# Kernel tuning notes

Hardware: AMD Instinct MI355X
Metric: run time of the kernel (lower is better)

The kernel has to match this reference:

```python
import jax, jax.numpy as jnp
import numpy as np

B, S, H = 8, 8192, 1024
CAPACITY_FACTOR = 0.5


def setup_inputs() -> dict:
    key = jax.random.key(0)
    ks = jax.random.split(key, 5)
    sc = lambda fan: np.float32(1.0 / np.sqrt(fan))
    return {
        "x": jax.random.normal(ks[0], (B, S, H), dtype=jnp.float32),
        # router: Linear(H, H//4) -> ReLU -> Linear(H//4, 1)
        "W1": jax.random.normal(ks[1], (H, H // 4), dtype=jnp.float32) * sc(H),
        "b1": jnp.zeros((H // 4,), dtype=jnp.float32),
        "W2": jax.random.normal(ks[2], (H // 4, 1), dtype=jnp.float32) * sc(H // 4),
        "b2": jnp.zeros((1,), dtype=jnp.float32),
        # external layer_fn realized as a dense layer: gelu(x @ Wl)
        "Wl": jax.random.normal(ks[3], (H, H), dtype=jnp.float32) * sc(H),
    }


def reference(x, W1, b1, W2, b2, Wl):
    # router scores [B, S, 1]
    scores = jax.nn.relu(jnp.einsum("bsh,hd->bsd", x, W1) + b1)
    scores = jnp.einsum("bsd,do->bso", scores, W2) + b2
    routing_weights = jax.nn.sigmoid(scores)  # [B, S, 1]

    # eval path: process only top-capacity tokens per batch row
    capacity = int(S * CAPACITY_FACTOR)
    _, top_idx = jax.lax.top_k(scores[..., 0], capacity)  # [B, C]

    selected = jnp.take_along_axis(x, top_idx[..., None], axis=1)  # [B, C, H]
    processed = jax.nn.gelu(jnp.einsum("bch,hd->bcd", selected, Wl))  # layer_fn

    batch_idx = jnp.arange(x.shape[0])[:, None]  # [B, 1]
    output = x.at[batch_idx, top_idx].set(processed)  # scatter back into clone of x
    return output, routing_weights
```

## Files before the change

### kernel.cpp

```cpp
#include <hip/hip_runtime.h>
#include <stdint.h>

#define B_   8
#define S_   8192
#define H_   1024
#define HQ_  256
#define CAP_ 4096
#define UCAP_ (S_-CAP_)
#define M_   (B_*CAP_)
#define EPSB 0.012f
#define LCAP 8192

using f32x4 = __attribute__((ext_vector_type(4))) float;
using s16x8 = __attribute__((ext_vector_type(8))) short;

__device__ __forceinline__ unsigned short f2bf(float f) {
  unsigned u = __float_as_uint(f);
  u += 0x7FFF + ((u >> 16) & 1);
  return (unsigned short)(u >> 16);
}
__device__ __forceinline__ float bf2f(unsigned short h) {
  return __uint_as_float(((unsigned)h) << 16);
}

__device__ __forceinline__ float gelu_f(float v) {
  float s = v + 0.044715f * v * v * v;
  float e = __expf(-1.5957691216057308f * s);
  return v * __builtin_amdgcn_rcpf(1.0f + e);
}

__device__ __forceinline__ unsigned mono(float f) {
  unsigned u = __float_as_uint(f);
  return (u & 0x80000000u) ? ~u : (u | 0x80000000u);
}
__device__ __forceinline__ float unmono(unsigned k) {
  unsigned u = (k & 0x80000000u) ? (k & 0x7fffffffu) : ~k;
  return __uint_as_float(u);
}

__device__ __forceinline__ void gload_lds16(const void* g, void* l) {
  __builtin_amdgcn_global_load_lds(
      (const __attribute__((address_space(1))) void*)(uintptr_t)g,
      (__attribute__((address_space(3))) void*)(uintptr_t)l,
      16, 0, 0);
}

__global__ __launch_bounds__(256) void prep_w1_kernel(
    const float* __restrict__ W1, unsigned short* __restrict__ w1t_hi) {
  __shared__ float tile[32][33];
  const int n0 = blockIdx.x * 32, k0 = blockIdx.y * 32;
  const int tx = threadIdx.x, ty = threadIdx.y;
  for (int i = ty; i < 32; i += 8) tile[i][tx] = W1[(size_t)(k0 + i) * HQ_ + n0 + tx];
  __syncthreads();
  for (int i = ty; i < 32; i += 8)
    w1t_hi[(size_t)(n0 + i) * H_ + k0 + tx] = f2bf(tile[tx][i]);
}

__global__ __launch_bounds__(512) void router_mfma_kernel(
    const float* __restrict__ x, const unsigned short* __restrict__ w1t_hi,
    const float* __restrict__ b1, const float* __restrict__ W2,
    const float* __restrict__ b2, float* __restrict__ scores,
    float* __restrict__ rw) {
  __shared__ __align__(16) unsigned short AsH[128 * 64];
  __shared__ __align__(16) unsigned short BsH[256 * 64];
  __shared__ float part[128][4];
  const int t = threadIdx.x;
  const int lane = t & 63, w = t >> 6;
  const int m0 = blockIdx.x * 128;
  const int wr = w >> 2, wc = w & 3;
  const int r16 = lane & 15, ks = lane >> 4;

  const float* aptr[4];
  int aso[4];
  #pragma unroll
  for (int u = 0; u < 4; ++u) {
    int idx = t + u * 512;
    int row = idx >> 4, q = idx & 15;
    aptr[u] = x + (size_t)(m0 + row) * H_ + q * 4;
    aso[u] = row * 64 + (((q >> 1) ^ (row & 7)) << 3) + (q & 1) * 4;
  }
  const unsigned short* bptr[4];
  int bdst[4];
  #pragma unroll
  for (int u = 0; u < 4; ++u) {
    int c0 = u * 512 + w * 64;
    int c = c0 + lane;
    int row = c >> 3, sl = c & 7;
    int slz = sl ^ (row & 7);
    bptr[u] = w1t_hi + (size_t)row * H_ + slz * 8;
    bdst[u] = c0 * 8;
  }

  f32x4 acc[4][4];
  #pragma unroll
  for (int i = 0; i < 4; ++i)
    #pragma unroll
    for (int j = 0; j < 4; ++j) acc[i][j] = (f32x4){0.f, 0.f, 0.f, 0.f};

  for (int k0 = 0; k0 < H_; k0 += 64) {
    float4 av[4];
    #pragma unroll
    for (int u = 0; u < 4; ++u) av[u] = *(const float4*)(aptr[u] + k0);
    #pragma unroll
    for (int u = 0; u < 4; ++u) gload_lds16(bptr[u] + k0, &BsH[bdst[u]]);
    #pragma unroll
    for (int u = 0; u < 4; ++u) {
      ushort4 hh;
      hh.x = f2bf(av[u].x); hh.y = f2bf(av[u].y);
      hh.z = f2bf(av[u].z); hh.w = f2bf(av[u].w);
      *(ushort4*)&AsH[aso[u]] = hh;
    }
    __syncthreads();
    #pragma unroll
    for (int kk = 0; kk < 2; ++kk) {
      const int g = kk * 4 + ks;
      s16x8 ah[4], bh[4];
      #pragma unroll
      for (int i = 0; i < 4; ++i) {
        int r = wr * 64 + i * 16 + r16;
        ah[i] = *(const s16x8*)&AsH[r * 64 + (g ^ (r & 7)) * 8];
      }
      #pragma unroll
      for (int j = 0; j < 4; ++j) {
        int r = wc * 64 + j * 16 + r16;
        bh[j] = *(const s16x8*)&BsH[r * 64 + (g ^ (r & 7)) * 8];
      }
      #pragma unroll
      for (int i = 0; i < 4; ++i)
        #pragma unroll
        for (int j = 0; j < 4; ++j)
          acc[i][j] = __builtin_amdgcn_mfma_f32_16x16x32_bf16(ah[i], bh[j], acc[i][j], 0, 0, 0);
    }
    __syncthreads();
  }

  float b1v[4], w2v[4];
  #pragma unroll
  for (int j = 0; j < 4; ++j) {
    int n = wc * 64 + j * 16 + r16;
    b1v[j] = b1[n]; w2v[j] = W2[n];
  }
  const int g4 = lane >> 4;
  #pragma unroll
  for (int i = 0; i < 4; ++i) {
    #pragma unroll
    for (int r = 0; r < 4; ++r) {
      float p = 0.f;
      #pragma unroll
      for (int j = 0; j < 4; ++j) {
        float h = acc[i][j][r] + b1v[j];
        h = fmaxf(h, 0.f);
        p = fmaf(h, w2v[j], p);
      }
      p += __shfl_xor(p, 1);
      p += __shfl_xor(p, 2);
      p += __shfl_xor(p, 4);
      p += __shfl_xor(p, 8);
      if (r16 == 0) part[wr * 64 + i * 16 + g4 * 4 + r][wc] = p;
    }
  }
  __syncthreads();
  if (t < 128) {
    float sc = part[t][0] + part[t][1] + part[t][2] + part[t][3] + b2[0];
    scores[m0 + t] = sc;
    rw[m0 + t] = 1.f / (1.f + expf(-sc));
  }
}

__global__ __launch_bounds__(1024) void select_kernel(
    const float* __restrict__ scores, float* __restrict__ thr) {
  __shared__ unsigned hist[2048];
  __shared__ unsigned sh_b, sh_gt;
  const int b = blockIdx.x;
  const int tid = threadIdx.x;
  const float* srow = scores + (size_t)b * S_;
  unsigned prefix = 0; int plen = 0; unsigned rank = CAP_;
  #pragma unroll
  for (int round = 0; round < 3; ++round) {
    const int nb = (round < 2) ? 11 : 10;
    hist[tid] = 0; hist[tid + 1024] = 0;
    __syncthreads();
    for (int i = tid; i < S_; i += 1024) {
      unsigned k = mono(srow[i]);
      if (plen == 0 || (k >> (32 - plen)) == prefix) {
        unsigned bucket = (k << plen) >> (32 - nb);
        atomicAdd(&hist[bucket], 1u);
      }
    }
    __syncthreads();
    for (int s = 1; s < 2048; s <<= 1) {
      unsigned t0 = (tid + s < 2048) ? hist[tid + s] : 0;
      unsigned t1 = (tid + 1024 + s < 2048) ? hist[tid + 1024 + s] : 0;
      __syncthreads();
      hist[tid] += t0; hist[tid + 1024] += t1;
      __syncthreads();
    }
    #pragma unroll
    for (int h = 0; h < 2; ++h) {
      int i = tid + h * 1024;
      unsigned ge = hist[i];
      unsigned gt = (i < 2047) ? hist[i + 1] : 0;
      if (gt < rank && rank <= ge) { sh_b = (unsigned)i; sh_gt = gt; }
    }
    __syncthreads();
    prefix = (prefix << nb) | sh_b;
    plen += nb;
    rank -= sh_gt;
    __syncthreads();
  }
  if (tid == 0) thr[b] = unmono(prefix);
}

__global__ __launch_bounds__(256) void band_kernel(
    const float* __restrict__ scores, const float* __restrict__ thr,
    int* __restrict__ list, int* __restrict__ count) {
  int i = blockIdx.x * 256 + threadIdx.x;
  float s = scores[i];
  int b = i >> 13;
  if (fabsf(s - thr[b]) <= EPSB) {
    int p = atomicAdd(count, 1);
    if (p < LCAP) list[p] = i;
  }
}

__global__ __launch_bounds__(256) void recompute_kernel(
    const float* __restrict__ x, const float* __restrict__ W1,
    const float* __restrict__ b1, const float* __restrict__ W2,
    const float* __restrict__ b2, const int* __restrict__ list,
    const int* __restrict__ count, float* __restrict__ scores,
    float* __restrict__ rw) {
  __shared__ float xr[4][H_];
  __shared__ float red[4][4];
  int n = *count; if (n > LCAP) n = LCAP;
  const int j = threadIdx.x;
  for (int base = blockIdx.x * 4; base < n; base += gridDim.x * 4) {
    int nt = n - base; if (nt > 4) nt = 4;
    for (int tt = 0; tt < 4; ++tt) {
      int tok = list[base + ((tt < nt) ? tt : 0)];
      const float* xrow = x + (size_t)tok * H_;
      for (int k = j; k < H_; k += 256) xr[tt][k] = xrow[k];
    }
    __syncthreads();
    float a0 = 0.f, a1 = 0.f, a2 = 0.f, a3 = 0.f;
    for (int k = 0; k < H_; ++k) {
      float wv = W1[(size_t)k * HQ_ + j];
      a0 = fmaf(xr[0][k], wv, a0);
      a1 = fmaf(xr[1][k], wv, a1);
      a2 = fmaf(xr[2][k], wv, a2);
      a3 = fmaf(xr[3][k], wv, a3);
    }
    float aa[4] = {a0, a1, a2, a3};
    #pragma unroll
    for (int tt = 0; tt < 4; ++tt) {
      float h = fmaxf(aa[tt] + b1[j], 0.f);
      float v = h * W2[j];
      v += __shfl_xor(v, 1);  v += __shfl_xor(v, 2);  v += __shfl_xor(v, 4);
      v += __shfl_xor(v, 8);  v += __shfl_xor(v, 16); v += __shfl_xor(v, 32);
      if ((j & 63) == 0) red[tt][j >> 6] = v;
    }
    __syncthreads();
    if (j < nt) {
      int tok = list[base + j];
      float sc = red[j][0] + red[j][1] + red[j][2] + red[j][3] + b2[0];
      scores[tok] = sc;
      rw[tok] = 1.f / (1.f + expf(-sc));
    }
    __syncthreads();
  }
}

__global__ __launch_bounds__(1024) void compact_kernel(
    const float* __restrict__ scores, const float* __restrict__ thr,
    int* __restrict__ comp, int* __restrict__ ucomp) {
  __shared__ int wc_eq[16], wc_sel[16], red[16];
  const int b = blockIdx.x;
  const float T = thr[b];
  const float* srow = scores + (size_t)b * S_;
  const int tid = threadIdx.x, lane = tid & 63, wid = tid >> 6;

  int cgt = 0;
  #pragma unroll
  for (int c = 0; c < 8; ++c) cgt += (srow[c * 1024 + tid] > T) ? 1 : 0;
  cgt += __shfl_xor(cgt, 1);  cgt += __shfl_xor(cgt, 2);  cgt += __shfl_xor(cgt, 4);
  cgt += __shfl_xor(cgt, 8);  cgt += __shfl_xor(cgt, 16); cgt += __shfl_xor(cgt, 32);
  if (lane == 0) red[wid] = cgt;
  __syncthreads();
  int cnt_gt = 0;
  #pragma unroll
  for (int i = 0; i < 16; ++i) cnt_gt += red[i];
  const int need = CAP_ - cnt_gt;

  int* crow = comp + b * CAP_;
  int* urow = ucomp + b * UCAP_;
  int sel_base = 0, unsel_base = 0, eq_base = 0;
  __syncthreads();
  for (int c = 0; c < 8; ++c) {
    int idx = c * 1024 + tid;
    float s = srow[idx];
    bool gt = s > T, eq = (s == T);
    unsigned long long meq = __ballot(eq);
    if (lane == 0) wc_eq[wid] = __popcll(meq);
    __syncthreads();
    int eq_off = eq_base, eq_tot = 0;
    #pragma unroll
    for (int w2 = 0; w2 < 16; ++w2) { if (w2 < wid) eq_off += wc_eq[w2]; eq_tot += wc_eq[w2]; }
    int eqpos = eq_off + __popcll(meq & ((1ull << lane) - 1));
    bool take = gt || (eq && eqpos < need);
    unsigned long long mt = __ballot(take);
    if (lane == 0) wc_sel[wid] = __popcll(mt);
    __syncthreads();
    int sel_off = sel_base, sel_tot = 0;
    #pragma unroll
    for (int w2 = 0; w2 < 16; ++w2) { if (w2 < wid) sel_off += wc_sel[w2]; sel_tot += wc_sel[w2]; }
    if (take) {
      crow[sel_off + __popcll(mt & ((1ull << lane) - 1))] = idx;
    } else {
      int un_off = unsel_base + wid * 64 - (sel_off - sel_base);
      urow[un_off + __popcll(~mt & ((1ull << lane) - 1))] = idx;
    }
    sel_base += sel_tot; unsel_base += 1024 - sel_tot; eq_base += eq_tot;
    __syncthreads();
  }
}

__global__ __launch_bounds__(256) void copy_unsel_kernel(
    const float* __restrict__ x, const int* __restrict__ ucomp,
    float* __restrict__ out) {
  int i = blockIdx.x;
  int b = i >> 12, r = i & (UCAP_ - 1);
  int token = ucomp[b * UCAP_ + r];
  size_t row = (size_t)b * S_ + token;
  const float4* src = (const float4*)(x + row * H_);
  float4* dst = (float4*)(out + row * H_);
  dst[threadIdx.x] = src[threadIdx.x];
}

__global__ __launch_bounds__(256) void wlt_kernel(
    const float* __restrict__ wl, unsigned short* __restrict__ wlt) {
  __shared__ float tile[32][33];
  const int x0 = blockIdx.x * 32, y0 = blockIdx.y * 32;
  const int tx = threadIdx.x, ty = threadIdx.y;
  for (int i = ty; i < 32; i += 8) tile[i][tx] = wl[(size_t)(y0 + i) * H_ + x0 + tx];
  __syncthreads();
  for (int i = ty; i < 32; i += 8)
    wlt[(size_t)(x0 + i) * H_ + y0 + tx] = f2bf(tile[tx][i]);
}

__global__ __launch_bounds__(256) void gather_cast_kernel(
    const float* __restrict__ x, const int* __restrict__ comp,
    unsigned short* __restrict__ xg) {
  int tid = blockIdx.x * 256 + threadIdx.x;
  int rowc = tid >> 8;
  int c4 = tid & 255;
  int b = rowc >> 12, cc = rowc & (CAP_ - 1);
  int token = comp[b * CAP_ + cc];
  float4 v = *(const float4*)&x[((size_t)(b * S_ + token)) * H_ + c4 * 4];
  ushort4 o;
  o.x = f2bf(v.x); o.y = f2bf(v.y); o.z = f2bf(v.z); o.w = f2bf(v.w);
  *(ushort4*)&xg[(size_t)rowc * H_ + c4 * 4] = o;
}

#define ISSUE_A(P, KT, BUF) do {                                               \
    int row_ = half * 128 + (P) * 32 + rr;                                     \
    int slz_ = sl ^ (row_ & 7);                                                \
    gload_lds16(xg + (size_t)(m0 + row_) * H_ + (KT) * 64 + slz_ * 8,          \
                &As[BUF][row_ * 64 + sl * 8]);                                 \
  } while (0)
#define ISSUE_B(P, KT, BUF) do {                                               \
    int row_ = half * 128 + (P) * 32 + rr;                                     \
    int slz_ = sl ^ (row_ & 7);                                                \
    gload_lds16(wlt + (size_t)(n0 + row_) * H_ + (KT) * 64 + slz_ * 8,         \
                &Bs[BUF][row_ * 64 + sl * 8]);                                 \
  } while (0)
#define MOE_PHASE(P, ISSUE, WAITSTR) do {                                      \
    s16x8 af[2][2];                                                            \
    _Pragma("unroll")                                                          \
    for (int i = 0; i < 2; ++i)                                                \
      _Pragma("unroll")                                                        \
      for (int kk = 0; kk < 2; ++kk) {                                         \
        int r_ = wr * 128 + (2 * (P) + i) * 16 + r16;                          \
        af[i][kk] = *(const s16x8*)&As[c_][r_ * 64 + ((kk * 4 + ks) ^ (r_ & 7)) * 8]; \
      }                                                                        \
    if ((P) == 0) {                                                            \
      _Pragma("unroll")                                                        \
      for (int j = 0; j < 4; ++j)                                              \
        _Pragma("unroll")                                                      \
        for (int kk = 0; kk < 2; ++kk) {                                       \
          int r_ = wc * 64 + j * 16 + r16;                                     \
          bfr[j][kk] = *(const s16x8*)&Bs[c_][r_ * 64 + ((kk * 4 + ks) ^ (r_ & 7)) * 8]; \
        }                                                                      \
    }                                                                          \
    ISSUE                                                                      \
    __builtin_amdgcn_s_barrier();                                              \
    asm volatile("s_waitcnt lgkmcnt(0)" ::: "memory");                         \
    __builtin_amdgcn_sched_barrier(0);                                         \
    __builtin_amdgcn_s_setprio(1);                                             \
    _Pragma("unroll")                                                          \
    for (int i = 0; i < 2; ++i)                                                \
      _Pragma("unroll")                                                        \
      for (int j = 0; j < 4; ++j)                                              \
        _Pragma("unroll")                                                      \
        for (int kk = 0; kk < 2; ++kk)                                         \
          acc[2 * (P) + i][j] = __builtin_amdgcn_mfma_f32_16x16x32_bf16(       \
              af[i][kk], bfr[j][kk], acc[2 * (P) + i][j], 0, 0, 0);            \
    __builtin_amdgcn_s_setprio(0);                                             \
    __builtin_amdgcn_sched_barrier(0);                                         \
    asm volatile("s_waitcnt " WAITSTR ::: "memory");                           \
    __builtin_amdgcn_s_barrier();                                              \
    __builtin_amdgcn_sched_barrier(0);                                         \
  } while (0)

__global__ __launch_bounds__(512, 1) void moe_gemm_kernel(
    const unsigned short* __restrict__ xg, const unsigned short* __restrict__ wlt,
    const int* __restrict__ comp, float* __restrict__ out) {
  __shared__ __align__(16) unsigned short As[2][256 * 64];
  __shared__ __align__(16) unsigned short Bs[2][256 * 64];
  __shared__ int toks[256];
  const int t = threadIdx.x;
  const int lane = t & 63, w = t >> 6;
  const int bid = blockIdx.x;
  const int xcd = bid & 7, wb = bid >> 3;
  const int m0 = (xcd * 16 + (wb >> 2)) * 256;
  const int n0 = (wb & 3) * 256;
  const int bb = m0 >> 12;
  if (t < 256) toks[t] = comp[bb * CAP_ + (m0 & (CAP_ - 1)) + t];
  const int wr = w >> 2, wc = w & 3;
  const int r16 = lane & 15, ks = lane >> 4;
  const int half = t >> 8, rr = (t >> 3) & 31, sl = t & 7;

  f32x4 acc[8][4];
  #pragma unroll
  for (int i = 0; i < 8; ++i)
    #pragma unroll
    for (int j = 0; j < 4; ++j) acc[i][j] = (f32x4){0.f, 0.f, 0.f, 0.f};

  ISSUE_B(0, 0, 0); ISSUE_B(1, 0, 0); ISSUE_B(2, 0, 0); ISSUE_B(3, 0, 0);
  ISSUE_A(0, 0, 0); ISSUE_A(1, 0, 0); ISSUE_A(2, 0, 0); ISSUE_A(3, 0, 0);
  asm volatile("s_waitcnt vmcnt(3)" ::: "memory");
  __syncthreads();

  for (int kt = 0; kt < 15; ++kt) {
    const int c_ = kt & 1, nb_ = c_ ^ 1;
    const int kn = kt + 1;
    s16x8 bfr[4][2];
    MOE_PHASE(0, { ISSUE_B(0, kn, nb_); ISSUE_B(1, kn, nb_); }, "vmcnt(4)");
    MOE_PHASE(1, { ISSUE_B(2, kn, nb_); ISSUE_B(3, kn, nb_); }, "vmcnt(5)");
    MOE_PHASE(2, { ISSUE_A(0, kn, nb_); ISSUE_A(1, kn, nb_); }, "vmcnt(6)");
    MOE_PHASE(3, { ISSUE_A(2, kn, nb_); ISSUE_A(3, kn, nb_); }, "vmcnt(3)");
  }
  {
    const int c_ = 1;
    s16x8 bfr[4][2];
    MOE_PHASE(0, {;}, "vmcnt(2)");
    MOE_PHASE(1, {;}, "vmcnt(1)");
    MOE_PHASE(2, {;}, "vmcnt(0)");
    MOE_PHASE(3, {;}, "vmcnt(63)");
  }

  const int g4 = lane >> 4;
  #pragma unroll
  for (int i = 0; i < 8; ++i) {
    #pragma unroll
    for (int r = 0; r < 4; ++r) {
      int rl = wr * 128 + i * 16 + g4 * 4 + r;
      int token = toks[rl];
      float* orow = out + ((size_t)(bb * S_ + token)) * H_ + n0 + wc * 64;
      #pragma unroll
      for (int j = 0; j < 4; ++j)
        orow[j * 16 + r16] = gelu_f(acc[i][j][r]);
    }
  }
}

extern "C" void kernel_launch(void* const* d_in, const int* in_sizes, int n_in,
                              void* d_out, int out_size, void* d_ws, size_t ws_size,
                              hipStream_t stream) {
  const float* x  = (const float*)d_in[0];
  const float* W1 = (const float*)d_in[1];
  const float* b1 = (const float*)d_in[2];
  const float* W2 = (const float*)d_in[3];
  const float* b2 = (const float*)d_in[4];
  const float* Wl = (const float*)d_in[5];
  float* out = (float*)d_out;
  float* rw  = out + (size_t)B_ * S_ * H_;

  char* ws = (char*)d_ws;
  float* scores        = (float*)ws;
  int*   comp          = (int*)(ws + (256 << 10));
  float* thr           = (float*)(ws + (384 << 10));
  int*   count         = (int*)(ws + (384 << 10) + 256);
  int*   list          = (int*)(ws + (384 << 10) + 512);
  int*   ucomp         = (int*)(ws + (448 << 10));
  unsigned short* wlt  = (unsigned short*)(ws + (1 << 20));
  unsigned short* xg   = (unsigned short*)(ws + (3 << 20));
  unsigned short* w1t_hi = xg;

  hipMemsetAsync(count, 0, sizeof(int), stream);
  hipLaunchKernelGGL(prep_w1_kernel, dim3(HQ_/32, H_/32), dim3(32, 8), 0, stream,
                     W1, w1t_hi);
  hipLaunchKernelGGL(router_mfma_kernel, dim3((B_*S_)/128), dim3(512), 0, stream,
                     x, w1t_hi, b1, W2, b2, scores, rw);
  hipLaunchKernelGGL(select_kernel, dim3(B_), dim3(1024), 0, stream, scores, thr);
  hipLaunchKernelGGL(band_kernel, dim3((B_*S_)/256), dim3(256), 0, stream,
                     scores, thr, list, count);
  hipLaunchKernelGGL(recompute_kernel, dim3(128), dim3(256), 0, stream,
                     x, W1, b1, W2, b2, list, count, scores, rw);
  hipLaunchKernelGGL(select_kernel, dim3(B_), dim3(1024), 0, stream, scores, thr);
  hipLaunchKernelGGL(compact_kernel, dim3(B_), dim3(1024), 0, stream,
                     scores, thr, comp, ucomp);
  hipLaunchKernelGGL(copy_unsel_kernel, dim3(B_*UCAP_), dim3(256), 0, stream,
                     x, ucomp, out);
  hipLaunchKernelGGL(wlt_kernel, dim3(H_/32, H_/32), dim3(32, 8), 0, stream, Wl, wlt);
  hipLaunchKernelGGL(gather_cast_kernel, dim3(M_*H_/4/256), dim3(256), 0, stream,
                     x, comp, xg);
  hipLaunchKernelGGL(moe_gemm_kernel, dim3((M_/256)*(H_/256)), dim3(512), 0, stream,
                     xg, wlt, comp, out);
}
```

Baseline: 398.4 us.

## Cast x to bf16 once and share it between router and gathered MoE GEMM

Adds a cast kernel that converts all of x to bf16 up front. The router GEMM then reads bf16 directly, with 256-row tiles and a double-buffered async-to-LDS pipeline reused from the MoE GEMM. The separate gather-cast kernel is removed: the MoE GEMM gathers selected token rows straight from the bf16 copy through per-row source pointers. This trades a full-tensor cast (a 128MB bf16 buffer in workspace) for halving the router's fp32 read traffic and dropping the intermediate gathered buffer.

Result: no change. 404.4 us (+1.5%).

```diff
diff --git a/kernel.cpp b/kernel.cpp
--- a/kernel.cpp
+++ b/kernel.cpp
@@ -45,6 +45,22 @@
       16, 0, 0);
 }
 
+__global__ __launch_bounds__(256) void cast_kernel(
+    const float* __restrict__ x, unsigned short* __restrict__ xbf) {
+  const size_t n8 = (size_t)B_ * S_ * H_ / 8;
+  size_t i = (size_t)blockIdx.x * 256 + threadIdx.x;
+  const size_t stride = (size_t)gridDim.x * 256;
+  for (; i < n8; i += stride) {
+    float4 v0 = *(const float4*)&x[i * 8];
+    float4 v1 = *(const float4*)&x[i * 8 + 4];
+    ushort4 o0, o1;
+    o0.x = f2bf(v0.x); o0.y = f2bf(v0.y); o0.z = f2bf(v0.z); o0.w = f2bf(v0.w);
+    o1.x = f2bf(v1.x); o1.y = f2bf(v1.y); o1.z = f2bf(v1.z); o1.w = f2bf(v1.w);
+    *(ushort4*)&xbf[i * 8] = o0;
+    *(ushort4*)&xbf[i * 8 + 4] = o1;
+  }
+}
+
 __global__ __launch_bounds__(256) void prep_w1_kernel(
     const float* __restrict__ W1, unsigned short* __restrict__ w1t_hi) {
   __shared__ float tile[32][33];
@@ -56,323 +72,7 @@
     w1t_hi[(size_t)(n0 + i) * H_ + k0 + tx] = f2bf(tile[tx][i]);
 }
 
-__global__ __launch_bounds__(512) void router_mfma_kernel(
-    const float* __restrict__ x, const unsigned short* __restrict__ w1t_hi,
-    const float* __restrict__ b1, const float* __restrict__ W2,
-    const float* __restrict__ b2, float* __restrict__ scores,
-    float* __restrict__ rw) {
-  __shared__ __align__(16) unsigned short AsH[128 * 64];
-  __shared__ __align__(16) unsigned short BsH[256 * 64];
-  __shared__ float part[128][4];
-  const int t = threadIdx.x;
-  const int lane = t & 63, w = t >> 6;
-  const int m0 = blockIdx.x * 128;
-  const int wr = w >> 2, wc = w & 3;
-  const int r16 = lane & 15, ks = lane >> 4;
-
-  const float* aptr[4];
-  int aso[4];
-  #pragma unroll
-  for (int u = 0; u < 4; ++u) {
-    int idx = t + u * 512;
-    int row = idx >> 4, q = idx & 15;
-    aptr[u] = x + (size_t)(m0 + row) * H_ + q * 4;
-    aso[u] = row * 64 + (((q >> 1) ^ (row & 7)) << 3) + (q & 1) * 4;
-  }
-  const unsigned short* bptr[4];
-  int bdst[4];
-  #pragma unroll
-  for (int u = 0; u < 4; ++u) {
-    int c0 = u * 512 + w * 64;
-    int c = c0 + lane;
-    int row = c >> 3, sl = c & 7;
-    int slz = sl ^ (row & 7);
-    bptr[u] = w1t_hi + (size_t)row * H_ + slz * 8;
-    bdst[u] = c0 * 8;
-  }
-
-  f32x4 acc[4][4];
-  #pragma unroll
-  for (int i = 0; i < 4; ++i)
-    #pragma unroll
-    for (int j = 0; j < 4; ++j) acc[i][j] = (f32x4){0.f, 0.f, 0.f, 0.f};
-
-  for (int k0 = 0; k0 < H_; k0 += 64) {
-    float4 av[4];
-    #pragma unroll
-    for (int u = 0; u < 4; ++u) av[u] = *(const float4*)(aptr[u] + k0);
-    #pragma unroll
-    for (int u = 0; u < 4; ++u) gload_lds16(bptr[u] + k0, &BsH[bdst[u]]);
-    #pragma unroll
-    for (int u = 0; u < 4; ++u) {
-      ushort4 hh;
-      hh.x = f2bf(av[u].x); hh.y = f2bf(av[u].y);
-      hh.z = f2bf(av[u].z); hh.w = f2bf(av[u].w);
-      *(ushort4*)&AsH[aso[u]] = hh;
-    }
-    __syncthreads();
-    #pragma unroll
-    for (int kk = 0; kk < 2; ++kk) {
-      const int g = kk * 4 + ks;
-      s16x8 ah[4], bh[4];
-      #pragma unroll
-      for (int i = 0; i < 4; ++i) {
-        int r = wr * 64 + i * 16 + r16;
-        ah[i] = *(const s16x8*)&AsH[r * 64 + (g ^ (r & 7)) * 8];
-      }
-      #pragma unroll
-      for (int j = 0; j < 4; ++j) {
-        int r = wc * 64 + j * 16 + r16;
-        bh[j] = *(const s16x8*)&BsH[r * 64 + (g ^ (r & 7)) * 8];
-      }
-      #pragma unroll
-      for (int i = 0; i < 4; ++i)
-        #pragma unroll
-        for (int j = 0; j < 4; ++j)
-          acc[i][j] = __builtin_amdgcn_mfma_f32_16x16x32_bf16(ah[i], bh[j], acc[i][j], 0, 0, 0);
-    }
-    __syncthreads();
-  }
-
-  float b1v[4], w2v[4];
-  #pragma unroll
-  for (int j = 0; j < 4; ++j) {
-    int n = wc * 64 + j * 16 + r16;
-    b1v[j] = b1[n]; w2v[j] = W2[n];
-  }
-  const int g4 = lane >> 4;
-  #pragma unroll
-  for (int i = 0; i < 4; ++i) {
-    #pragma unroll
-    for (int r = 0; r < 4; ++r) {
-      float p = 0.f;
-      #pragma unroll
-      for (int j = 0; j < 4; ++j) {
-        float h = acc[i][j][r] + b1v[j];
-        h = fmaxf(h, 0.f);
-        p = fmaf(h, w2v[j], p);
-      }
-      p += __shfl_xor(p, 1);
-      p += __shfl_xor(p, 2);
-      p += __shfl_xor(p, 4);
-      p += __shfl_xor(p, 8);
-      if (r16 == 0) part[wr * 64 + i * 16 + g4 * 4 + r][wc] = p;
-    }
-  }
-  __syncthreads();
-  if (t < 128) {
-    float sc = part[t][0] + part[t][1] + part[t][2] + part[t][3] + b2[0];
-    scores[m0 + t] = sc;
-    rw[m0 + t] = 1.f / (1.f + expf(-sc));
-  }
-}
-
-__global__ __launch_bounds__(1024) void select_kernel(
-    const float* __restrict__ scores, float* __restrict__ thr) {
-  __shared__ unsigned hist[2048];
-  __shared__ unsigned sh_b, sh_gt;
-  const int b = blockIdx.x;
-  const int tid = threadIdx.x;
-  const float* srow = scores + (size_t)b * S_;
-  unsigned prefix = 0; int plen = 0; unsigned rank = CAP_;
-  #pragma unroll
-  for (int round = 0; round < 3; ++round) {
-    const int nb = (round < 2) ? 11 : 10;
-    hist[tid] = 0; hist[tid + 1024] = 0;
-    __syncthreads();
-    for (int i = tid; i < S_; i += 1024) {
-      unsigned k = mono(srow[i]);
-      if (plen == 0 || (k >> (32 - plen)) == prefix) {
-        unsigned bucket = (k << plen) >> (32 - nb);
-        atomicAdd(&hist[bucket], 1u);
-      }
-    }
-    __syncthreads();
-    for (int s = 1; s < 2048; s <<= 1) {
-      unsigned t0 = (tid + s < 2048) ? hist[tid + s] : 0;
-      unsigned t1 = (tid + 1024 + s < 2048) ? hist[tid + 1024 + s] : 0;
-      __syncthreads();
-      hist[tid] += t0; hist[tid + 1024] += t1;
-      __syncthreads();
-    }
-    #pragma unroll
-    for (int h = 0; h < 2; ++h) {
-      int i = tid + h * 1024;
-      unsigned ge = hist[i];
-      unsigned gt = (i < 2047) ? hist[i + 1] : 0;
-      if (gt < rank && rank <= ge) { sh_b = (unsigned)i; sh_gt = gt; }
-    }
-    __syncthreads();
-    prefix = (prefix << nb) | sh_b;
-    plen += nb;
-    rank -= sh_gt;
-    __syncthreads();
-  }
-  if (tid == 0) thr[b] = unmono(prefix);
-}
-
-__global__ __launch_bounds__(256) void band_kernel(
-    const float* __restrict__ scores, const float* __restrict__ thr,
-    int* __restrict__ list, int* __restrict__ count) {
-  int i = blockIdx.x * 256 + threadIdx.x;
-  float s = scores[i];
-  int b = i >> 13;
-  if (fabsf(s - thr[b]) <= EPSB) {
-    int p = atomicAdd(count, 1);
-    if (p < LCAP) list[p] = i;
-  }
-}
-
-__global__ __launch_bounds__(256) void recompute_kernel(
-    const float* __restrict__ x, const float* __restrict__ W1,
-    const float* __restrict__ b1, const float* __restrict__ W2,
-    const float* __restrict__ b2, const int* __restrict__ list,
-    const int* __restrict__ count, float* __restrict__ scores,
-    float* __restrict__ rw) {
-  __shared__ float xr[4][H_];
-  __shared__ float red[4][4];
-  int n = *count; if (n > LCAP) n = LCAP;
-  const int j = threadIdx.x;
-  for (int base = blockIdx.x * 4; base < n; base += gridDim.x * 4) {
-    int nt = n - base; if (nt > 4) nt = 4;
-    for (int tt = 0; tt < 4; ++tt) {
-      int tok = list[base + ((tt < nt) ? tt : 0)];
-      const float* xrow = x + (size_t)tok * H_;
-      for (int k = j; k < H_; k += 256) xr[tt][k] = xrow[k];
-    }
-    __syncthreads();
-    float a0 = 0.f, a1 = 0.f, a2 = 0.f, a3 = 0.f;
-    for (int k = 0; k < H_; ++k) {
-      float wv = W1[(size_t)k * HQ_ + j];
-      a0 = fmaf(xr[0][k], wv, a0);
-      a1 = fmaf(xr[1][k], wv, a1);
-      a2 = fmaf(xr[2][k], wv, a2);
-      a3 = fmaf(xr[3][k], wv, a3);
-    }
-    float aa[4] = {a0, a1, a2, a3};
-    #pragma unroll
-    for (int tt = 0; tt < 4; ++tt) {
-      float h = fmaxf(aa[tt] + b1[j], 0.f);
-      float v = h * W2[j];
-      v += __shfl_xor(v, 1);  v += __shfl_xor(v, 2);  v += __shfl_xor(v, 4);
-      v += __shfl_xor(v, 8);  v += __shfl_xor(v, 16); v += __shfl_xor(v, 32);
-      if ((j & 63) == 0) red[tt][j >> 6] = v;
-    }
-    __syncthreads();
-    if (j < nt) {
-      int tok = list[base + j];
-      float sc = red[j][0] + red[j][1] + red[j][2] + red[j][3] + b2[0];
-      scores[tok] = sc;
-      rw[tok] = 1.f / (1.f + expf(-sc));
-    }
-    __syncthreads();
-  }
-}
-
-__global__ __launch_bounds__(1024) void compact_kernel(
-    const float* __restrict__ scores, const float* __restrict__ thr,
-    int* __restrict__ comp, int* __restrict__ ucomp) {
-  __shared__ int wc_eq[16], wc_sel[16], red[16];
-  const int b = blockIdx.x;
-  const float T = thr[b];
-  const float* srow = scores + (size_t)b * S_;
-  const int tid = threadIdx.x, lane = tid & 63, wid = tid >> 6;
-
-  int cgt = 0;
-  #pragma unroll
-  for (int c = 0; c < 8; ++c) cgt += (srow[c * 1024 + tid] > T) ? 1 : 0;
-  cgt += __shfl_xor(cgt, 1);  cgt += __shfl_xor(cgt, 2);  cgt += __shfl_xor(cgt, 4);
-  cgt += __shfl_xor(cgt, 8);  cgt += __shfl_xor(cgt, 16); cgt += __shfl_xor(cgt, 32);
-  if (lane == 0) red[wid] = cgt;
-  __syncthreads();
-  int cnt_gt = 0;
-  #pragma unroll
-  for (int i = 0; i < 16; ++i) cnt_gt += red[i];
-  const int need = CAP_ - cnt_gt;
-
-  int* crow = comp + b * CAP_;
-  int* urow = ucomp + b * UCAP_;
-  int sel_base = 0, unsel_base = 0, eq_base = 0;
-  __syncthreads();
-  for (int c = 0; c < 8; ++c) {
-    int idx = c * 1024 + tid;
-    float s = srow[idx];
-    bool gt = s > T, eq = (s == T);
-    unsigned long long meq = __ballot(eq);
-    if (lane == 0) wc_eq[wid] = __popcll(meq);
-    __syncthreads();
-    int eq_off = eq_base, eq_tot = 0;
-    #pragma unroll
-    for (int w2 = 0; w2 < 16; ++w2) { if (w2 < wid) eq_off += wc_eq[w2]; eq_tot += wc_eq[w2]; }
-    int eqpos = eq_off + __popcll(meq & ((1ull << lane) - 1));
-    bool take = gt || (eq && eqpos < need);
-    unsigned long long mt = __ballot(take);
-    if (lane == 0) wc_sel[wid] = __popcll(mt);
-    __syncthreads();
-    int sel_off = sel_base, sel_tot = 0;
-    #pragma unroll
-    for (int w2 = 0; w2 < 16; ++w2) { if (w2 < wid) sel_off += wc_sel[w2]; sel_tot += wc_sel[w2]; }
-    if (take) {
-      crow[sel_off + __popcll(mt & ((1ull << lane) - 1))] = idx;
-    } else {
-      int un_off = unsel_base + wid * 64 - (sel_off - sel_base);
-      urow[un_off + __popcll(~mt & ((1ull << lane) - 1))] = idx;
-    }
-    sel_base += sel_tot; unsel_base += 1024 - sel_tot; eq_base += eq_tot;
-    __syncthreads();
-  }
-}
-
-__global__ __launch_bounds__(256) void copy_unsel_kernel(
-    const float* __restrict__ x, const int* __restrict__ ucomp,
-    float* __restrict__ out) {
-  int i = blockIdx.x;
-  int b = i >> 12, r = i & (UCAP_ - 1);
-  int token = ucomp[b * UCAP_ + r];
-  size_t row = (size_t)b * S_ + token;
-  const float4* src = (const float4*)(x + row * H_);
-  float4* dst = (float4*)(out + row * H_);
-  dst[threadIdx.x] = src[threadIdx.x];
-}
-
-__global__ __launch_bounds__(256) void wlt_kernel(
-    const float* __restrict__ wl, unsigned short* __restrict__ wlt) {
-  __shared__ float tile[32][33];
-  const int x0 = blockIdx.x * 32, y0 = blockIdx.y * 32;
-  const int tx = threadIdx.x, ty = threadIdx.y;
-  for (int i = ty; i < 32; i += 8) tile[i][tx] = wl[(size_t)(y0 + i) * H_ + x0 + tx];
-  __syncthreads();
-  for (int i = ty; i < 32; i += 8)
-    wlt[(size_t)(x0 + i) * H_ + y0 + tx] = f2bf(tile[tx][i]);
-}
-
-__global__ __launch_bounds__(256) void gather_cast_kernel(
-    const float* __restrict__ x, const int* __restrict__ comp,
-    unsigned short* __restrict__ xg) {
-  int tid = blockIdx.x * 256 + threadIdx.x;
-  int rowc = tid >> 8;
-  int c4 = tid & 255;
-  int b = rowc >> 12, cc = rowc & (CAP_ - 1);
-  int token = comp[b * CAP_ + cc];
-  float4 v = *(const float4*)&x[((size_t)(b * S_ + token)) * H_ + c4 * 4];
-  ushort4 o;
-  o.x = f2bf(v.x); o.y = f2bf(v.y); o.z = f2bf(v.z); o.w = f2bf(v.w);
-  *(ushort4*)&xg[(size_t)rowc * H_ + c4 * 4] = o;
-}
-
-#define ISSUE_A(P, KT, BUF) do {                                               \
-    int row_ = half * 128 + (P) * 32 + rr;                                     \
-    int slz_ = sl ^ (row_ & 7);                                                \
-    gload_lds16(xg + (size_t)(m0 + row_) * H_ + (KT) * 64 + slz_ * 8,          \
-                &As[BUF][row_ * 64 + sl * 8]);                                 \
-  } while (0)
-#define ISSUE_B(P, KT, BUF) do {                                               \
-    int row_ = half * 128 + (P) * 32 + rr;                                     \
-    int slz_ = sl ^ (row_ & 7);                                                \
-    gload_lds16(wlt + (size_t)(n0 + row_) * H_ + (KT) * 64 + slz_ * 8,         \
-                &Bs[BUF][row_ * 64 + sl * 8]);                                 \
-  } while (0)
-#define MOE_PHASE(P, ISSUE, WAITSTR) do {                                      \
+#define GPHASE(P, ISSUE, WAITSTR) do {                                         \
     s16x8 af[2][2];                                                            \
     _Pragma("unroll")                                                          \
     for (int i = 0; i < 2; ++i)                                                \
@@ -410,8 +110,288 @@
     __builtin_amdgcn_sched_barrier(0);                                         \
   } while (0)
 
+#define RIA(P, KT, BUF) do {                                                   \
+    int row_ = half * 128 + (P) * 32 + rr;                                     \
+    int slz_ = sl ^ (row_ & 7);                                                \
+    gload_lds16(xbf + (size_t)(m0 + row_) * H_ + (KT) * 64 + slz_ * 8,         \
+                &As[BUF][row_ * 64 + sl * 8]);                                 \
+  } while (0)
+#define RIB(P, KT, BUF) do {                                                   \
+    int row_ = half * 128 + (P) * 32 + rr;                                     \
+    int slz_ = sl ^ (row_ & 7);                                                \
+    gload_lds16(w1t_hi + (size_t)row_ * H_ + (KT) * 64 + slz_ * 8,             \
+                &Bs[BUF][row_ * 64 + sl * 8]);                                 \
+  } while (0)
+
+__global__ __launch_bounds__(512, 1) void router_mfma_kernel(
+    const unsigned short* __restrict__ xbf, const unsigned short* __restrict__ w1t_hi,
+    const float* __restrict__ b1, const float* __restrict__ W2,
+    const float* __restrict__ b2, float* __restrict__ scores,
+    float* __restrict__ rw) {
+  __shared__ __align__(16) unsigned short As[2][256 * 64];
+  __shared__ __align__(16) unsigned short Bs[2][256 * 64];
+  __shared__ float part[256][4];
+  const int t = threadIdx.x;
+  const int lane = t & 63, w = t >> 6;
+  const int m0 = blockIdx.x * 256;
+  const int wr = w >> 2, wc = w & 3;
+  const int r16 = lane & 15, ks = lane >> 4;
+  const int half = t >> 8, rr = (t >> 3) & 31, sl = t & 7;
+
+  f32x4 acc[8][4];
+  #pragma unroll
+  for (int i = 0; i < 8; ++i)
+    #pragma unroll
+    for (int j = 0; j < 4; ++j) acc[i][j] = (f32x4){0.f, 0.f, 0.f, 0.f};
+
+  RIB(0, 0, 0); RIB(1, 0, 0); RIB(2, 0, 0); RIB(3, 0, 0);
+  RIA(0, 0, 0); RIA(1, 0, 0); RIA(2, 0, 0); RIA(3, 0, 0);
+  asm volatile("s_waitcnt vmcnt(3)" ::: "memory");
+  __syncthreads();
+
+  for (int kt = 0; kt < 15; ++kt) {
+    const int c_ = kt & 1, nb_ = c_ ^ 1;
+    const int kn = kt + 1;
+    s16x8 bfr[4][2];
+    GPHASE(0, { RIB(0, kn, nb_); RIB(1, kn, nb_); }, "vmcnt(4)");
+    GPHASE(1, { RIB(2, kn, nb_); RIB(3, kn, nb_); }, "vmcnt(5)");
+    GPHASE(2, { RIA(0, kn, nb_); RIA(1, kn, nb_); }, "vmcnt(6)");
+    GPHASE(3, { RIA(2, kn, nb_); RIA(3, kn, nb_); }, "vmcnt(3)");
+  }
+  {
+    const int c_ = 1;
+    s16x8 bfr[4][2];
+    GPHASE(0, {;}, "vmcnt(2)");
+    GPHASE(1, {;}, "vmcnt(1)");
+    GPHASE(2, {;}, "vmcnt(0)");
+    GPHASE(3, {;}, "vmcnt(63)");
+  }
+
+  float b1v[4], w2v[4];
+  #pragma unroll
+  for (int j = 0; j < 4; ++j) {
+    int n = wc * 64 + j * 16 + r16;
+    b1v[j] = b1[n]; w2v[j] = W2[n];
+  }
+  const int g4 = lane >> 4;
+  #pragma unroll
+  for (int i = 0; i < 8; ++i) {
+    #pragma unroll
+    for (int r = 0; r < 4; ++r) {
+      float p = 0.f;
+      #pragma unroll
+      for (int j = 0; j < 4; ++j) {
+        float h = acc[i][j][r] + b1v[j];
+        h = fmaxf(h, 0.f);
+        p = fmaf(h, w2v[j], p);
+      }
+      p += __shfl_xor(p, 1);
+      p += __shfl_xor(p, 2);
+      p += __shfl_xor(p, 4);
+      p += __shfl_xor(p, 8);
+      if (r16 == 0) part[wr * 128 + i * 16 + g4 * 4 + r][wc] = p;
+    }
+  }
+  __syncthreads();
+  if (t < 256) {
+    float sc = part[t][0] + part[t][1] + part[t][2] + part[t][3] + b2[0];
+    scores[m0 + t] = sc;
+    rw[m0 + t] = 1.f / (1.f + expf(-sc));
+  }
+}
+
+__global__ __launch_bounds__(1024) void select_kernel(
+    const float* __restrict__ scores, float* __restrict__ thr) {
+  __shared__ unsigned hist[2048];
+  __shared__ unsigned sh_b, sh_gt;
+  const int b = blockIdx.x;
+  const int tid = threadIdx.x;
+  const float* srow = scores + (size_t)b * S_;
+  unsigned prefix = 0; int plen = 0; unsigned rank = CAP_;
+  #pragma unroll
+  for (int round = 0; round < 3; ++round) {
+    const int nb = (round < 2) ? 11 : 10;
+    hist[tid] = 0; hist[tid + 1024] = 0;
+    __syncthreads();
+    for (int i = tid; i < S_; i += 1024) {
+      unsigned k = mono(srow[i]);
+      if (plen == 0 || (k >> (32 - plen)) == prefix) {
+        unsigned bucket = (k << plen) >> (32 - nb);
+        atomicAdd(&hist[bucket], 1u);
+      }
+    }
+    __syncthreads();
+    for (int s = 1; s < 2048; s <<= 1) {
+      unsigned t0 = (tid + s < 2048) ? hist[tid + s] : 0;
+      unsigned t1 = (tid + 1024 + s < 2048) ? hist[tid + 1024 + s] : 0;
+      __syncthreads();
+      hist[tid] += t0; hist[tid + 1024] += t1;
+      __syncthreads();
+    }
+    #pragma unroll
+    for (int h = 0; h < 2; ++h) {
+      int i = tid + h * 1024;
+      unsigned ge = hist[i];
+      unsigned gt = (i < 2047) ? hist[i + 1] : 0;
+      if (gt < rank && rank <= ge) { sh_b = (unsigned)i; sh_gt = gt; }
+    }
+    __syncthreads();
+    prefix = (prefix << nb) | sh_b;
+    plen += nb;
+    rank -= sh_gt;
+    __syncthreads();
+  }
+  if (tid == 0) thr[b] = unmono(prefix);
+}
+
+__global__ __launch_bounds__(256) void band_kernel(
+    const float* __restrict__ scores, const float* __restrict__ thr,
+    int* __restrict__ list, int* __restrict__ count) {
+  int i = blockIdx.x * 256 + threadIdx.x;
+  float s = scores[i];
+  int b = i >> 13;
+  if (fabsf(s - thr[b]) <= EPSB) {
+    int p = atomicAdd(count, 1);
+    if (p < LCAP) list[p] = i;
+  }
+}
+
+__global__ __launch_bounds__(256) void recompute_kernel(
+    const float* __restrict__ x, const float* __restrict__ W1,
+    const float* __restrict__ b1, const float* __restrict__ W2,
+    const float* __restrict__ b2, const int* __restrict__ list,
+    const int* __restrict__ count, float* __restrict__ scores,
+    float* __restrict__ rw) {
+  __shared__ float xr[4][H_];
+  __shared__ float red[4][4];
+  int n = *count; if (n > LCAP) n = LCAP;
+  const int j = threadIdx.x;
+  for (int base = blockIdx.x * 4; base < n; base += gridDim.x * 4) {
+    int nt = n - base; if (nt > 4) nt = 4;
+    for (int tt = 0; tt < 4; ++tt) {
+      int tok = list[base + ((tt < nt) ? tt : 0)];
+      const float* xrow = x + (size_t)tok * H_;
+      for (int k = j; k < H_; k += 256) xr[tt][k] = xrow[k];
+    }
+    __syncthreads();
+    float a0 = 0.f, a1 = 0.f, a2 = 0.f, a3 = 0.f;
+    for (int k = 0; k < H_; ++k) {
+      float wv = W1[(size_t)k * HQ_ + j];
+      a0 = fmaf(xr[0][k], wv, a0);
+      a1 = fmaf(xr[1][k], wv, a1);
+      a2 = fmaf(xr[2][k], wv, a2);
+      a3 = fmaf(xr[3][k], wv, a3);
+    }
+    float aa[4] = {a0, a1, a2, a3};
+    #pragma unroll
+    for (int tt = 0; tt < 4; ++tt) {
+      float h = fmaxf(aa[tt] + b1[j], 0.f);
+      float v = h * W2[j];
+      v += __shfl_xor(v, 1);  v += __shfl_xor(v, 2);  v += __shfl_xor(v, 4);
+      v += __shfl_xor(v, 8);  v += __shfl_xor(v, 16); v += __shfl_xor(v, 32);
+      if ((j & 63) == 0) red[tt][j >> 6] = v;
+    }
+    __syncthreads();
+    if (j < nt) {
+      int tok = list[base + j];
+      float sc = red[j][0] + red[j][1] + red[j][2] + red[j][3] + b2[0];
+      scores[tok] = sc;
+      rw[tok] = 1.f / (1.f + expf(-sc));
+    }
+    __syncthreads();
+  }
+}
+
+__global__ __launch_bounds__(1024) void compact_kernel(
+    const float* __restrict__ scores, const float* __restrict__ thr,
+    int* __restrict__ comp, int* __restrict__ ucomp) {
+  __shared__ int wc_eq[16], wc_sel[16], red[16];
+  const int b = blockIdx.x;
+  const float T = thr[b];
+  const float* srow = scores + (size_t)b * S_;
+  const int tid = threadIdx.x, lane = tid & 63, wid = tid >> 6;
+
+  int cgt = 0;
+  #pragma unroll
+  for (int c = 0; c < 8; ++c) cgt += (srow[c * 1024 + tid] > T) ? 1 : 0;
+  cgt += __shfl_xor(cgt, 1);  cgt += __shfl_xor(cgt, 2);  cgt += __shfl_xor(cgt, 4);
+  cgt += __shfl_xor(cgt, 8);  cgt += __shfl_xor(cgt, 16); cgt += __shfl_xor(cgt, 32);
+  if (lane == 0) red[wid] = cgt;
+  __syncthreads();
+  int cnt_gt = 0;
+  #pragma unroll
+  for (int i = 0; i < 16; ++i) cnt_gt += red[i];
+  const int need = CAP_ - cnt_gt;
+
+  int* crow = comp + b * CAP_;
+  int* urow = ucomp + b * UCAP_;
+  int sel_base = 0, unsel_base = 0, eq_base = 0;
+  __syncthreads();
+  for (int c = 0; c < 8; ++c) {
+    int idx = c * 1024 + tid;
+    float s = srow[idx];
+    bool gt = s > T, eq = (s == T);
+    unsigned long long meq = __ballot(eq);
+    if (lane == 0) wc_eq[wid] = __popcll(meq);
+    __syncthreads();
+    int eq_off = eq_base, eq_tot = 0;
+    #pragma unroll
+    for (int w2 = 0; w2 < 16; ++w2) { if (w2 < wid) eq_off += wc_eq[w2]; eq_tot += wc_eq[w2]; }
+    int eqpos = eq_off + __popcll(meq & ((1ull << lane) - 1));
+    bool take = gt || (eq && eqpos < need);
+    unsigned long long mt = __ballot(take);
+    if (lane == 0) wc_sel[wid] = __popcll(mt);
+    __syncthreads();
+    int sel_off = sel_base, sel_tot = 0;
+    #pragma unroll
+    for (int w2 = 0; w2 < 16; ++w2) { if (w2 < wid) sel_off += wc_sel[w2]; sel_tot += wc_sel[w2]; }
+    if (take) {
+      crow[sel_off + __popcll(mt & ((1ull << lane) - 1))] = idx;
+    } else {
+      int un_off = unsel_base + wid * 64 - (sel_off - sel_base);
+      urow[un_off + __popcll(~mt & ((1ull << lane) - 1))] = idx;
+    }
+    sel_base += sel_tot; unsel_base += 1024 - sel_tot; eq_base += eq_tot;
+    __syncthreads();
+  }
+}
+
+__global__ __launch_bounds__(256) void copy_unsel_kernel(
+    const float* __restrict__ x, const int* __restrict__ ucomp,
+    float* __restrict__ out) {
+  int i = blockIdx.x;
+  int b = i >> 12, r = i & (UCAP_ - 1);
+  int token = ucomp[b * UCAP_ + r];
+  size_t row = (size_t)b * S_ + token;
+  const float4* src = (const float4*)(x + row * H_);
+  float4* dst = (float4*)(out + row * H_);
+  dst[threadIdx.x] = src[threadIdx.x];
+}
+
+__global__ __launch_bounds__(256) void wlt_kernel(
+    const float* __restrict__ wl, unsigned short* __restrict__ wlt) {
+  __shared__ float tile[32][33];
+  const int x0 = blockIdx.x * 32, y0 = blockIdx.y * 32;
+  const int tx = threadIdx.x, ty = threadIdx.y;
+  for (int i = ty; i < 32; i += 8) tile[i][tx] = wl[(size_t)(y0 + i) * H_ + x0 + tx];
+  __syncthreads();
+  for (int i = ty; i < 32; i += 8)
+    wlt[(size_t)(x0 + i) * H_ + y0 + tx] = f2bf(tile[tx][i]);
+}
+
+#define MIA(P, KT, BUF) do {                                                   \
+    int row_ = half * 128 + (P) * 32 + rr;                                     \
+    gload_lds16(aSrc[P] + (KT) * 64, &As[BUF][row_ * 64 + sl * 8]);            \
+  } while (0)
+#define MIB(P, KT, BUF) do {                                                   \
+    int row_ = half * 128 + (P) * 32 + rr;                                     \
+    int slz_ = sl ^ (row_ & 7);                                                \
+    gload_lds16(wlt + (size_t)(n0 + row_) * H_ + (KT) * 64 + slz_ * 8,         \
+                &Bs[BUF][row_ * 64 + sl * 8]);                                 \
+  } while (0)
+
 __global__ __launch_bounds__(512, 1) void moe_gemm_kernel(
-    const unsigned short* __restrict__ xg, const unsigned short* __restrict__ wlt,
+    const unsigned short* __restrict__ xbf, const unsigned short* __restrict__ wlt,
     const int* __restrict__ comp, float* __restrict__ out) {
   __shared__ __align__(16) unsigned short As[2][256 * 64];
   __shared__ __align__(16) unsigned short Bs[2][256 * 64];
@@ -427,6 +407,15 @@
   const int wr = w >> 2, wc = w & 3;
   const int r16 = lane & 15, ks = lane >> 4;
   const int half = t >> 8, rr = (t >> 3) & 31, sl = t & 7;
+  __syncthreads();
+
+  const unsigned short* aSrc[4];
+  #pragma unroll
+  for (int P = 0; P < 4; ++P) {
+    int row_ = half * 128 + P * 32 + rr;
+    int slz_ = sl ^ (row_ & 7);
+    aSrc[P] = xbf + ((size_t)(bb * S_ + toks[row_])) * H_ + slz_ * 8;
+  }
 
   f32x4 acc[8][4];
   #pragma unroll
@@ -434,27 +423,28 @@
     #pragma unroll
     for (int j = 0; j < 4; ++j) acc[i][j] = (f32x4){0.f, 0.f, 0.f, 0.f};
 
-  ISSUE_B(0, 0, 0); ISSUE_B(1, 0, 0); ISSUE_B(2, 0, 0); ISSUE_B(3, 0, 0);
-  ISSUE_A(0, 0, 0); ISSUE_A(1, 0, 0); ISSUE_A(2, 0, 0); ISSUE_A(3, 0, 0);
+  MIB(0, 0, 0); MIB(1, 0, 0); MIB(2, 0, 0); MIB(3, 0, 0);
+  MIA(0, 0, 0); MIA(1, 0, 0); MIA(2, 0, 0); MIA(3, 0, 0);
   asm volatile("s_waitcnt vmcnt(3)" ::: "memory");
-  __syncthreads();
+  __builtin_amdgcn_s_barrier();
+  __builtin_amdgcn_sched_barrier(0);
 
   for (int kt = 0; kt < 15; ++kt) {
     const int c_ = kt & 1, nb_ = c_ ^ 1;
     const int kn = kt + 1;
     s16x8 bfr[4][2];
-    MOE_PHASE(0, { ISSUE_B(0, kn, nb_); ISSUE_B(1, kn, nb_); }, "vmcnt(4)");
-    MOE_PHASE(1, { ISSUE_B(2, kn, nb_); ISSUE_B(3, kn, nb_); }, "vmcnt(5)");
-    MOE_PHASE(2, { ISSUE_A(0, kn, nb_); ISSUE_A(1, kn, nb_); }, "vmcnt(6)");
-    MOE_PHASE(3, { ISSUE_A(2, kn, nb_); ISSUE_A(3, kn, nb_); }, "vmcnt(3)");
+    GPHASE(0, { MIB(0, kn, nb_); MIB(1, kn, nb_); }, "vmcnt(4)");
+    GPHASE(1, { MIB(2, kn, nb_); MIB(3, kn, nb_); }, "vmcnt(5)");
+    GPHASE(2, { MIA(0, kn, nb_); MIA(1, kn, nb_); }, "vmcnt(6)");
+    GPHASE(3, { MIA(2, kn, nb_); MIA(3, kn, nb_); }, "vmcnt(3)");
   }
   {
     const int c_ = 1;
     s16x8 bfr[4][2];
-    MOE_PHASE(0, {;}, "vmcnt(2)");
-    MOE_PHASE(1, {;}, "vmcnt(1)");
-    MOE_PHASE(2, {;}, "vmcnt(0)");
-    MOE_PHASE(3, {;}, "vmcnt(63)");
+    GPHASE(0, {;}, "vmcnt(2)");
+    GPHASE(1, {;}, "vmcnt(1)");
+    GPHASE(2, {;}, "vmcnt(0)");
+    GPHASE(3, {;}, "vmcnt(63)");
   }
 
   const int g4 = lane >> 4;
@@ -492,14 +482,15 @@
   int*   list          = (int*)(ws + (384 << 10) + 512);
   int*   ucomp         = (int*)(ws + (448 << 10));
   unsigned short* wlt  = (unsigned short*)(ws + (1 << 20));
-  unsigned short* xg   = (unsigned short*)(ws + (3 << 20));
-  unsigned short* w1t_hi = xg;
+  unsigned short* xbf  = (unsigned short*)(ws + (3 << 20));
+  unsigned short* w1t_hi = (unsigned short*)(ws + ((size_t)131 << 20));
 
   hipMemsetAsync(count, 0, sizeof(int), stream);
   hipLaunchKernelGGL(prep_w1_kernel, dim3(HQ_/32, H_/32), dim3(32, 8), 0, stream,
                      W1, w1t_hi);
-  hipLaunchKernelGGL(router_mfma_kernel, dim3((B_*S_)/128), dim3(512), 0, stream,
-                     x, w1t_hi, b1, W2, b2, scores, rw);
+  hipLaunchKernelGGL(cast_kernel, dim3(2048), dim3(256), 0, stream, x, xbf);
+  hipLaunchKernelGGL(router_mfma_kernel, dim3((B_*S_)/256), dim3(512), 0, stream,
+                     xbf, w1t_hi, b1, W2, b2, scores, rw);
   hipLaunchKernelGGL(select_kernel, dim3(B_), dim3(1024), 0, stream, scores, thr);
   hipLaunchKernelGGL(band_kernel, dim3((B_*S_)/256), dim3(256), 0, stream,
                      scores, thr, list, count);
@@ -511,8 +502,6 @@
   hipLaunchKernelGGL(copy_unsel_kernel, dim3(B_*UCAP_), dim3(256), 0, stream,
                      x, ucomp, out);
   hipLaunchKernelGGL(wlt_kernel, dim3(H_/32, H_/32), dim3(32, 8), 0, stream, Wl, wlt);
-  hipLaunchKernelGGL(gather_cast_kernel, dim3(M_*H_/4/256), dim3(256), 0, stream,
-                     x, comp, xg);
   hipLaunchKernelGGL(moe_gemm_kernel, dim3((M_/256)*(H_/256)), dim3(512), 0, stream,
-                     xg, wlt, comp, out);
-}
+                     xbf, wlt, comp, out);
+}
```
